# Kernel tuning notes

Measured on AMD Instinct MI355X. Metric: run time of the kernel, lower is better.

## Reference

```python
import jax, jax.numpy as jnp
import numpy as np

N_E = 16384          # codebook size (power of 2)
E_DIM = 14           # log2(N_E)
BETA = 0.25
ENTROPY_LOSS_RATIO = 0.1
TEMPERATURE = 0.01
EPS = 1e-5
USAGE_BUF = 65536


def make_codebook():
    codes = jnp.arange(N_E)
    bits = (codes[:, None] & (2 ** jnp.arange(E_DIM))) != 0  # [N_E, E_DIM] big-endian bits
    return bits.astype(jnp.float32) * 2.0 - 1.0


def setup_inputs() -> dict:
    key = jax.random.key(0)
    z = jax.random.normal(key, (4, E_DIM, 32, 32), dtype=jnp.float32)  # b d h w
    codebook = make_codebook()                                         # [N_E, E_DIM]
    codebook_used = jnp.zeros((USAGE_BUF,), dtype=jnp.int32)           # ring buffer
    return {"z": z, "codebook": codebook, "codebook_used": codebook_used}


def reference(z, codebook, codebook_used):
    b, d, h, w = z.shape
    # b d h w -> b n c d  (num_codebooks c = 1)
    zr = jnp.transpose(z, (0, 2, 3, 1)).reshape(b, h * w, 1, d)

    # lookup-free sign quantization
    q = jnp.where(zr > 0, jnp.float32(1.0), jnp.float32(-1.0)).astype(zr.dtype)
    bit_weights = (2 ** jnp.arange(d)).astype(jnp.int32)
    indices = jnp.sum((q > 0).astype(jnp.int32) * bit_weights, axis=-1)  # b n c

    # entropy auxiliary loss over codebook affinities
    logits = 2.0 * jnp.einsum('bncd,jd->bncj', zr, codebook)  # [b,n,1,N_E]
    scaled = logits / TEMPERATURE
    probs = jax.nn.softmax(scaled, axis=-1)
    log_probs = jax.nn.log_softmax(scaled + EPS, axis=-1)
    avg_probs = jnp.mean(probs, axis=(0, 1, 2))                       # [N_E]
    avg_entropy = -jnp.sum(avg_probs * jnp.log(avg_probs + EPS))
    sample_entropy = jnp.mean(-jnp.sum(probs * log_probs, axis=-1))
    entropy_aux_loss = ENTROPY_LOSS_RATIO * (1.0 * sample_entropy - 1.0 * avg_entropy)

    # commitment loss (quantized detached)
    commit_loss = BETA * jnp.mean((zr - jax.lax.stop_gradient(q)) ** 2)

    # straight-through estimator
    quantized = zr + jax.lax.stop_gradient(q - zr)
    quantized = jnp.transpose(quantized.reshape(b, h, w, d), (0, 3, 1, 2))  # b d h w

    # codebook usage ring-buffer update + unique-count via histogram
    idx_flat = indices.reshape(-1)
    cur_len = idx_flat.shape[0]
    buf = jnp.concatenate([codebook_used[cur_len:], idx_flat.astype(codebook_used.dtype)])
    counts = jnp.zeros((USAGE_BUF,), jnp.int32).at[buf].add(1)
    codebook_usage = jnp.sum(counts > 0).astype(jnp.float32) / N_E

    return quantized, commit_loss, entropy_aux_loss, codebook_usage, idx_flat
```

## Files before the change

kernel.cpp:

```cpp
#include <hip/hip_runtime.h>
#include <math.h>


static constexpr int NE     = 16384;
static constexpr int EDIM   = 14;
static constexpr int SEP    = 15;
static constexpr int NTOK   = 4096;
static constexpr int ZELEMS = 57344;
static constexpr int P      = 128;
static constexpr int TPB    = 32;
static constexpr int RING_BLOCKS = (65536 - NTOK) / 1024;

static constexpr unsigned POISON    = 0xAAAAAAAAu;
static constexpr unsigned CTR_LAST  = POISON + 63u;

static constexpr size_t FL_OFF  = (size_t)P * 65536;
static constexpr size_t ACC_OFF = FL_OFF + 65536;
static constexpr size_t CNT_OFF = ACC_OFF + 16;

__global__ __launch_bounds__(256) void mega_kernel(
    const float* __restrict__ z, const int* __restrict__ used,
    float* __restrict__ out, float* __restrict__ partial,
    int* __restrict__ flags, float* __restrict__ acc)
{
    const int tid = threadIdx.x;
    const int bid = blockIdx.x;

    if (bid >= P) {
        const int i0 = NTOK + (bid - P) * 1024 + tid * 4;
        int4 v = *(const int4*)&used[i0];
        flags[v.x & (NE - 1)] = 1;
        flags[v.y & (NE - 1)] = 1;
        flags[v.z & (NE - 1)] = 1;
        flags[v.w & (NE - 1)] = 1;
        return;
    }

    __shared__ float sEA[TPB * 128], sEB[TPB * 128];
    __shared__ float se[TPB * SEP], szv[TPB * SEP];
    __shared__ float sEsc[TPB], sC[TPB], sH[TPB];
    __shared__ int   sBits[TPB];

    const int t0    = bid * TPB;
    const int b     = t0 >> 10;
    const int zbase = b * 14336 + (t0 & 1023);

    for (int p = tid; p < EDIM * TPB; p += 256) {
        const int k  = p >> 5;
        const int tt = p & (TPB - 1);
        const int ga = zbase + k * 1024 + tt;
        float zv = z[ga];
        out[ga] = zv > 0.f ? 1.f : -1.f;
        szv[tt * SEP + k] = zv;
        se [tt * SEP + k] = __expf(-400.f * fabsf(zv));
    }
    __syncthreads();

    if (tid < TPB) {
        const int tt = tid;
        float c = 0.f, h = 0.f, lzr = 0.f;
        int bits = 0;
        #pragma unroll
        for (int k = 0; k < EDIM; ++k) {
            float zv = szv[tt * SEP + k];
            float e  = se [tt * SEP + k];
            int bit = zv > 0.f;
            bits |= bit << k;
            float q = bit ? 1.f : -1.f;
            float d = zv - q;
            c += d * d;
            float u  = 400.f * fabsf(zv);
            float l1 = log1pf(e);
            lzr += l1;
            h += l1 + u * e / (1.f + e);
        }
        sBits[tt] = bits;
        sEsc[tt]  = __expf(-lzr);
        sC[tt] = c; sH[tt] = h;
        out[ZELEMS + 3 + t0 + tt] = (float)bits;
        flags[bits] = 1;
    }
    __syncthreads();

    if (tid == 64) {
        float c = 0.f, h = 0.f;
        #pragma unroll
        for (int i = 0; i < TPB; ++i) { c += sC[i]; h += sH[i]; }
        atomicAdd(&acc[0], c);
        atomicAdd(&acc[1], h);
    }

    {
        const int tt = tid >> 3;
        const int j0 = (tid & 7) * 16;
        float ee[EDIM];
        #pragma unroll
        for (int k = 0; k < EDIM; ++k) ee[k] = se[tt * SEP + k];
        const int   bits = sBits[tt];
        const float esc  = sEsc[tt];
        for (int c = 0; c < 16; ++c) {
            const int j = j0 + c;
            float pa = 1.f, pb = 1.f;
            #pragma unroll
            for (int k = 0; k < 7; ++k) {
                pa *= (((j >> k) & 1) != ((bits >> k) & 1))       ? ee[k]     : 1.f;
                pb *= (((j >> k) & 1) != ((bits >> (k + 7)) & 1)) ? ee[k + 7] : 1.f;
            }
            sEA[tt * 128 + j] = pa;
            sEB[tt * 128 + j] = pb * esc;
        }
    }
    __syncthreads();

    const int tx = tid & 15, ty = tid >> 4;
    const int jlo0 = tx * 8, jhi0 = ty * 8;
    float a8[8][8] = {};
    for (int tt = 0; tt < TPB; ++tt) {
        float4 a0 = *(const float4*)&sEA[tt * 128 + jlo0];
        float4 a1 = *(const float4*)&sEA[tt * 128 + jlo0 + 4];
        float4 b0 = *(const float4*)&sEB[tt * 128 + jhi0];
        float4 b1 = *(const float4*)&sEB[tt * 128 + jhi0 + 4];
        float ea[8] = {a0.x, a0.y, a0.z, a0.w, a1.x, a1.y, a1.z, a1.w};
        float eb[8] = {b0.x, b0.y, b0.z, b0.w, b1.x, b1.y, b1.z, b1.w};
        #pragma unroll
        for (int jj = 0; jj < 8; ++jj)
            #pragma unroll
            for (int ii = 0; ii < 8; ++ii) a8[jj][ii] += eb[jj] * ea[ii];
    }

    float* dst = partial + (size_t)bid * 16384;
    #pragma unroll
    for (int jj = 0; jj < 8; ++jj) {
        *(float4*)&dst[(jhi0 + jj) * 128 + jlo0] =
            make_float4(a8[jj][0], a8[jj][1], a8[jj][2], a8[jj][3]);
        *(float4*)&dst[(jhi0 + jj) * 128 + jlo0 + 4] =
            make_float4(a8[jj][4], a8[jj][5], a8[jj][6], a8[jj][7]);
    }
}

__global__ __launch_bounds__(256) void reduce_kernel(
    const float* __restrict__ partial, const int* __restrict__ flags,
    float* __restrict__ acc, unsigned int* __restrict__ counter,
    float* __restrict__ out)
{
    const int tid = threadIdx.x;
    const int j = blockIdx.x * 256 + tid;

    float s0 = 0.f, s1 = 0.f, s2 = 0.f, s3 = 0.f;
    for (int p = 0; p < P; p += 4) {
        s0 += partial[(size_t)(p + 0) * 16384 + j];
        s1 += partial[(size_t)(p + 1) * 16384 + j];
        s2 += partial[(size_t)(p + 2) * 16384 + j];
        s3 += partial[(size_t)(p + 3) * 16384 + j];
    }
    float a = (s0 + s1 + s2 + s3) * (1.0f / 4096.0f);
    float v_ent = a * logf(a + 1e-5f);
    float v_cnt = (flags[j] == 1) ? 1.f : 0.f;

    __shared__ float red[2][256];
    red[0][tid] = v_ent; red[1][tid] = v_cnt;
    __syncthreads();
    for (int off = 128; off > 0; off >>= 1) {
        if (tid < off) { red[0][tid] += red[0][tid + off]; red[1][tid] += red[1][tid + off]; }
        __syncthreads();
    }
    if (tid == 0) {
        atomicAdd(&acc[2], red[0][0]);
        atomicAdd(&acc[3], red[1][0]);
        __threadfence();
        unsigned int old = atomicAdd(counter, 1u);
        if (old == CTR_LAST) {
            __threadfence();
            float c   = atomicAdd(&acc[0], 0.f);
            float h   = atomicAdd(&acc[1], 0.f);
            float ent = atomicAdd(&acc[2], 0.f);
            float cnt = atomicAdd(&acc[3], 0.f);
            float avg_entropy    = -ent;
            float sample_entropy = h * (1.0f / 4096.0f);
            out[ZELEMS + 0] = 0.25f * c * (1.0f / (float)ZELEMS);
            out[ZELEMS + 1] = 0.1f * (sample_entropy - avg_entropy);
            out[ZELEMS + 2] = cnt * (1.0f / (float)NE);
        }
    }
}

extern "C" void kernel_launch(void* const* d_in, const int* in_sizes, int n_in,
                              void* d_out, int out_size, void* d_ws, size_t ws_size,
                              hipStream_t stream)
{
    const float* z    = (const float*)d_in[0];
    const int*   used = (const int*)d_in[2];
    float* out = (float*)d_out;
    char*  ws  = (char*)d_ws;

    float*        partial = (float*)ws;
    int*          flags   = (int*)  (ws + FL_OFF);
    float*        acc     = (float*)(ws + ACC_OFF);
    unsigned int* counter = (unsigned int*)(ws + CNT_OFF);

    mega_kernel<<<P + RING_BLOCKS, 256, 0, stream>>>(z, used, out, partial, flags, acc);
    reduce_kernel<<<64, 256, 0, stream>>>(partial, flags, acc, counter, out);
}
```

Measured before the change: 92.04 us.

## Split reduce over partition groups across 256 blocks; use float2 accumulators in outer product

The reduce kernel now launches 256 blocks, each covering 64 codebook entries. Its four waves each sum a quarter of the 128 partial slices, and the results are combined in shared memory and then with a wave shuffle. This spreads the 8 MB partial-buffer read over more CUs to raise memory-level parallelism, at the cost of four times as many global atomics on the accumulators and counter. The mega kernel's 8x8 outer-product accumulation is restated with float2 pairs, presumably to encourage packed FMA (v_pk_fma_f32) code generation.

```diff
diff --git a/kernel.cpp b/kernel.cpp
--- a/kernel.cpp
+++ b/kernel.cpp
@@ -10,9 +10,10 @@
 static constexpr int P      = 128;
 static constexpr int TPB    = 32;
 static constexpr int RING_BLOCKS = (65536 - NTOK) / 1024;
+static constexpr int RB     = 256;
 
 static constexpr unsigned POISON    = 0xAAAAAAAAu;
-static constexpr unsigned CTR_LAST  = POISON + 63u;
+static constexpr unsigned CTR_LAST  = POISON + (unsigned)RB - 1u;
 
 static constexpr size_t FL_OFF  = (size_t)P * 65536;
 static constexpr size_t ACC_OFF = FL_OFF + 65536;
@@ -114,27 +115,30 @@
 
     const int tx = tid & 15, ty = tid >> 4;
     const int jlo0 = tx * 8, jhi0 = ty * 8;
-    float a8[8][8] = {};
+    float2 a8[8][4] = {};
     for (int tt = 0; tt < TPB; ++tt) {
-        float4 a0 = *(const float4*)&sEA[tt * 128 + jlo0];
-        float4 a1 = *(const float4*)&sEA[tt * 128 + jlo0 + 4];
+        const float2* pa = (const float2*)&sEA[tt * 128 + jlo0];
+        float2 e0 = pa[0], e1 = pa[1], e2 = pa[2], e3 = pa[3];
         float4 b0 = *(const float4*)&sEB[tt * 128 + jhi0];
         float4 b1 = *(const float4*)&sEB[tt * 128 + jhi0 + 4];
-        float ea[8] = {a0.x, a0.y, a0.z, a0.w, a1.x, a1.y, a1.z, a1.w};
         float eb[8] = {b0.x, b0.y, b0.z, b0.w, b1.x, b1.y, b1.z, b1.w};
         #pragma unroll
-        for (int jj = 0; jj < 8; ++jj)
-            #pragma unroll
-            for (int ii = 0; ii < 8; ++ii) a8[jj][ii] += eb[jj] * ea[ii];
+        for (int jj = 0; jj < 8; ++jj) {
+            const float bb = eb[jj];
+            a8[jj][0].x += bb * e0.x; a8[jj][0].y += bb * e0.y;
+            a8[jj][1].x += bb * e1.x; a8[jj][1].y += bb * e1.y;
+            a8[jj][2].x += bb * e2.x; a8[jj][2].y += bb * e2.y;
+            a8[jj][3].x += bb * e3.x; a8[jj][3].y += bb * e3.y;
+        }
     }
 
     float* dst = partial + (size_t)bid * 16384;
     #pragma unroll
     for (int jj = 0; jj < 8; ++jj) {
         *(float4*)&dst[(jhi0 + jj) * 128 + jlo0] =
-            make_float4(a8[jj][0], a8[jj][1], a8[jj][2], a8[jj][3]);
+            make_float4(a8[jj][0].x, a8[jj][0].y, a8[jj][1].x, a8[jj][1].y);
         *(float4*)&dst[(jhi0 + jj) * 128 + jlo0 + 4] =
-            make_float4(a8[jj][4], a8[jj][5], a8[jj][6], a8[jj][7]);
+            make_float4(a8[jj][2].x, a8[jj][2].y, a8[jj][3].x, a8[jj][3].y);
     }
 }
 
@@ -144,42 +148,50 @@
     float* __restrict__ out)
 {
     const int tid = threadIdx.x;
-    const int j = blockIdx.x * 256 + tid;
-
+    const int jl  = tid & 63;
+    const int pg  = tid >> 6;
+    const int j   = blockIdx.x * 64 + jl;
+
+    const float* base = partial + (size_t)pg * (32u * 16384u) + j;
     float s0 = 0.f, s1 = 0.f, s2 = 0.f, s3 = 0.f;
-    for (int p = 0; p < P; p += 4) {
-        s0 += partial[(size_t)(p + 0) * 16384 + j];
-        s1 += partial[(size_t)(p + 1) * 16384 + j];
-        s2 += partial[(size_t)(p + 2) * 16384 + j];
-        s3 += partial[(size_t)(p + 3) * 16384 + j];
-    }
-    float a = (s0 + s1 + s2 + s3) * (1.0f / 4096.0f);
-    float v_ent = a * logf(a + 1e-5f);
-    float v_cnt = (flags[j] == 1) ? 1.f : 0.f;
-
-    __shared__ float red[2][256];
-    red[0][tid] = v_ent; red[1][tid] = v_cnt;
-    __syncthreads();
-    for (int off = 128; off > 0; off >>= 1) {
-        if (tid < off) { red[0][tid] += red[0][tid + off]; red[1][tid] += red[1][tid + off]; }
-        __syncthreads();
-    }
-    if (tid == 0) {
-        atomicAdd(&acc[2], red[0][0]);
-        atomicAdd(&acc[3], red[1][0]);
-        __threadfence();
-        unsigned int old = atomicAdd(counter, 1u);
-        if (old == CTR_LAST) {
+    #pragma unroll
+    for (int p = 0; p < 32; p += 4) {
+        s0 += base[(size_t)(p + 0) * 16384];
+        s1 += base[(size_t)(p + 1) * 16384];
+        s2 += base[(size_t)(p + 2) * 16384];
+        s3 += base[(size_t)(p + 3) * 16384];
+    }
+    __shared__ float red[4][64];
+    red[pg][jl] = (s0 + s1) + (s2 + s3);
+    __syncthreads();
+
+    if (tid < 64) {
+        float a = (red[0][jl] + red[1][jl] + red[2][jl] + red[3][jl])
+                  * (1.0f / 4096.0f);
+        float v_ent = a * logf(a + 1e-5f);
+        float v_cnt = (flags[j] == 1) ? 1.f : 0.f;
+        #pragma unroll
+        for (int off = 32; off > 0; off >>= 1) {
+            v_ent += __shfl_down(v_ent, off, 64);
+            v_cnt += __shfl_down(v_cnt, off, 64);
+        }
+        if (tid == 0) {
+            atomicAdd(&acc[2], v_ent);
+            atomicAdd(&acc[3], v_cnt);
             __threadfence();
-            float c   = atomicAdd(&acc[0], 0.f);
-            float h   = atomicAdd(&acc[1], 0.f);
-            float ent = atomicAdd(&acc[2], 0.f);
-            float cnt = atomicAdd(&acc[3], 0.f);
-            float avg_entropy    = -ent;
-            float sample_entropy = h * (1.0f / 4096.0f);
-            out[ZELEMS + 0] = 0.25f * c * (1.0f / (float)ZELEMS);
-            out[ZELEMS + 1] = 0.1f * (sample_entropy - avg_entropy);
-            out[ZELEMS + 2] = cnt * (1.0f / (float)NE);
+            unsigned int old = atomicAdd(counter, 1u);
+            if (old == CTR_LAST) {
+                __threadfence();
+                float c   = atomicAdd(&acc[0], 0.f);
+                float h   = atomicAdd(&acc[1], 0.f);
+                float ent = atomicAdd(&acc[2], 0.f);
+                float cnt = atomicAdd(&acc[3], 0.f);
+                float avg_entropy    = -ent;
+                float sample_entropy = h * (1.0f / 4096.0f);
+                out[ZELEMS + 0] = 0.25f * c * (1.0f / (float)ZELEMS);
+                out[ZELEMS + 1] = 0.1f * (sample_entropy - avg_entropy);
+                out[ZELEMS + 2] = cnt * (1.0f / (float)NE);
+            }
         }
     }
 }
@@ -199,5 +211,5 @@
     unsigned int* counter = (unsigned int*)(ws + CNT_OFF);
 
     mega_kernel<<<P + RING_BLOCKS, 256, 0, stream>>>(z, used, out, partial, flags, acc);
-    reduce_kernel<<<64, 256, 0, stream>>>(partial, flags, acc, counter, out);
+    reduce_kernel<<<RB, 256, 0, stream>>>(partial, flags, acc, counter, out);
 }
```

New measurement: 86.22 us. -6.3%, faster.
